# Performance work log

Hardware: AMD Instinct MI355X
Metric: run time of the kernel (lower is better)

The kernel has to match this reference:

```python
import jax, jax.numpy as jnp
import numpy as np

B, S, M, D, H = 2, 2048, 512, 1024, 16
HD = D // H      # head dim 64
KVC = D // 16    # MLA kv compression dim 64
QC = D // 32     # MLA q compression dim 32
RD = HD          # retrieval (qk) head dim 64
LOOKBACK = 8     # cross_window
EPS = 1e-6


def rmsnorm(x, w):
    return x * jax.lax.rsqrt(jnp.mean(x * x, axis=-1, keepdims=True) + EPS) * w


def setup_inputs():
    key = jax.random.key(0)
    ks = jax.random.split(key, 20)
    g = lambda i, shape: jax.random.normal(ks[i], shape, jnp.float32) * 0.02
    return {
        "x": jax.random.normal(ks[0], (B, S, D), jnp.float32),
        "memory": jax.random.normal(ks[1], (B, M, D), jnp.float32),
        "seg_ids": jnp.sort(jax.random.randint(ks[2], (B, S), 0, M), axis=-1),
        "norm1_w": jnp.ones((D,), jnp.float32),
        "W_dq": g(3, (D, QC)),
        "W_uq": g(4, (QC, H * RD)),
        "W_dkv": g(5, (D, KVC)),
        "W_uk": g(6, (KVC, H * RD)),
        "W_uv": g(7, (KVC, H * HD)),
        "W_o_self": g(8, (H * HD, D)),
        "norm2_w": jnp.ones((D,), jnp.float32),
        "W_q_c": g(9, (D, D)),
        "W_k_c": g(10, (D, D)),
        "W_v_c": g(11, (D, D)),
        "W_o_c": g(12, (D, D)),
        "norm3_w": jnp.ones((D,), jnp.float32),
        "W_gate": g(13, (D, 4 * D)),
        "W_up": g(14, (D, 4 * D)),
        "W_down": g(15, (4 * D, D)),
    }


def reference(x, memory, seg_ids, norm1_w, W_dq, W_uq, W_dkv, W_uk, W_uv,
              W_o_self, norm2_w, W_q_c, W_k_c, W_v_c, W_o_c, norm3_w,
              W_gate, W_up, W_down):
    # ---- MLA causal self-attention (low-rank compressed q/kv) ----
    h = rmsnorm(x, norm1_w)
    q = ((h @ W_dq) @ W_uq).reshape(B, S, H, RD)
    c_kv = h @ W_dkv                                  # [B,S,KVC]
    k = (c_kv @ W_uk).reshape(B, S, H, RD)
    v = (c_kv @ W_uv).reshape(B, S, H, HD)
    scores = jnp.einsum('bihd,bjhd->bhij', q, k) / np.float32(np.sqrt(RD))
    causal = jnp.tril(jnp.ones((S, S), bool))
    scores = jnp.where(causal, scores, -jnp.inf)
    attn = jax.nn.softmax(scores, axis=-1)
    o = jnp.einsum('bhij,bjhd->bihd', attn, v).reshape(B, S, H * HD)
    x = x + o @ W_o_self
    # ---- segment sliding-window cross-attention ----
    h = rmsnorm(x, norm2_w)
    qc = (h @ W_q_c).reshape(B, S, H, HD)
    kc = (memory @ W_k_c).reshape(B, M, H, HD)
    vc = (memory @ W_v_c).reshape(B, M, H, HD)
    sc = jnp.einsum('bihd,bjhd->bhij', qc, kc) / np.float32(np.sqrt(HD))
    kv_pos = jnp.arange(M)
    seg = seg_ids[:, :, None]                          # [B,S,1]
    allowed = (kv_pos[None, None, :] <= seg) & (kv_pos[None, None, :] >= seg - LOOKBACK)
    sc = jnp.where(allowed[:, None, :, :], sc, -jnp.inf)
    ac = jax.nn.softmax(sc, axis=-1)
    oc = jnp.einsum('bhij,bjhd->bihd', ac, vc).reshape(B, S, D)
    x = x + oc @ W_o_c
    # ---- SwiGLU FFN ----
    h = rmsnorm(x, norm3_w)
    x = x + (jax.nn.silu(h @ W_gate) * (h @ W_up)) @ W_down
    return x
```

## Files before the change

### kernel.cpp

```cpp
#include <hip/hip_runtime.h>
#include <stdint.h>

typedef unsigned short U16;
typedef __bf16 bf16x8 __attribute__((ext_vector_type(8)));
typedef unsigned short us8 __attribute__((ext_vector_type(8)));
typedef float f32x4 __attribute__((ext_vector_type(4)));

__device__ __forceinline__ U16 f2bf(float f) {
    unsigned u = __builtin_bit_cast(unsigned, f);
    unsigned r = (u + 0x7fff + ((u >> 16) & 1)) >> 16;
    return (U16)r;
}
__device__ __forceinline__ U16 f2bf_fast(float f) {
    return (U16)((__builtin_bit_cast(unsigned, f) + 0x8000u) >> 16);
}
__device__ __forceinline__ float bf2f(U16 v) {
    return __builtin_bit_cast(float, (unsigned)v << 16);
}
__device__ __forceinline__ bf16x8 ld8(const U16* p) { return __builtin_bit_cast(bf16x8, *(const us8*)p); }

__device__ __forceinline__ void async16(const U16* g, U16* l) {
    auto* gp = (const __attribute__((address_space(1))) U16*)g;
    auto* lp = (__attribute__((address_space(3))) U16*)(uintptr_t)(uint32_t)(uintptr_t)l;
    __builtin_amdgcn_global_load_lds(gp, lp, 16, 0, 0);
}

struct WEnt { const float* src; U16* dst; int K, N, Kpad, Npad, koff, noff, tiles; };
struct WTable { WEnt e[13]; };

__global__ __launch_bounds__(256) void wtrans_all(WTable t) {
    int bx = blockIdx.x, ei = 0;
    while (bx >= t.e[ei].tiles) { bx -= t.e[ei].tiles; ei++; }
    const WEnt E = t.e[ei];
    const int ntn = E.Npad >> 5;
    const int n0 = (bx % ntn) * 32, k0 = (bx / ntn) * 32;
    __shared__ float tile[32][33];
    const int tx = threadIdx.x & 31, ty = threadIdx.x >> 5;
#pragma unroll
    for (int i = 0; i < 4; i++) {
        int kk = k0 + ty + i * 8, n = n0 + tx;
        int k = kk - E.koff;
        float v = (k >= 0 && k < E.K && n < E.N) ? E.src[(size_t)k * E.N + n] : 0.f;
        tile[ty + i * 8][tx] = v;
    }
    __syncthreads();
#pragma unroll
    for (int i = 0; i < 4; i++) {
        int n = n0 + ty + i * 8, kk = k0 + tx;
        E.dst[(size_t)(E.noff + n) * E.Kpad + kk] = f2bf(tile[tx][ty + i * 8]);
    }
}

__global__ __launch_bounds__(256) void f2bf_k(const float* __restrict__ in, U16* __restrict__ out, int n) {
    int i = (blockIdx.x * 256 + threadIdx.x) * 4;
    if (i < n) {
        float4 v = *(const float4*)(in + i);
        out[i + 0] = f2bf(v.x); out[i + 1] = f2bf(v.y);
        out[i + 2] = f2bf(v.z); out[i + 3] = f2bf(v.w);
    }
}

__global__ __launch_bounds__(256) void cq_reduce(const float* __restrict__ p, U16* __restrict__ out) {
    int i = (blockIdx.x * 256 + threadIdx.x) * 4;
    const float4 a = *(const float4*)(p + i);
    const float4 b = *(const float4*)(p + 524288 + i);
    const float4 c = *(const float4*)(p + 2 * 524288 + i);
    const float4 d = *(const float4*)(p + 3 * 524288 + i);
    out[i + 0] = f2bf(a.x + b.x + c.x + d.x);
    out[i + 1] = f2bf(a.y + b.y + c.y + d.y);
    out[i + 2] = f2bf(a.z + b.z + c.z + d.z);
    out[i + 3] = f2bf(a.w + b.w + c.w + d.w);
}

__global__ __launch_bounds__(256) void rmsnorm_k(const float* __restrict__ x, const float* __restrict__ w,
                                                 U16* __restrict__ h) {
    const int row = blockIdx.x, tid = threadIdx.x;
    const float4 v = *(const float4*)(x + (size_t)row * 1024 + tid * 4);
    float ss = v.x * v.x + v.y * v.y + v.z * v.z + v.w * v.w;
#pragma unroll
    for (int o = 32; o > 0; o >>= 1) ss += __shfl_xor(ss, o);
    __shared__ float red[4];
    if ((tid & 63) == 0) red[tid >> 6] = ss;
    __syncthreads();
    float tot = red[0] + red[1] + red[2] + red[3];
    float sc = rsqrtf(tot * (1.0f / 1024.0f) + 1e-6f);
    const float4 wv = *(const float4*)(w + tid * 4);
    U16* hp = h + (size_t)row * 1024 + tid * 4;
    hp[0] = f2bf(v.x * sc * wv.x); hp[1] = f2bf(v.y * sc * wv.y);
    hp[2] = f2bf(v.z * sc * wv.z); hp[3] = f2bf(v.w * sc * wv.w);
}

__global__ __launch_bounds__(256) void qkuv_gemm(const U16* __restrict__ A, const U16* __restrict__ Wuqk,
                                                 const U16* __restrict__ Wuv,
                                                 U16* __restrict__ qkb, U16* __restrict__ vt) {
    __shared__ __align__(16) U16 As[2][128 * 32];
    __shared__ __align__(16) U16 Bs[2][128 * 32];
    __shared__ __align__(16) U16 Ts[4][64 * 80];
    const int tid = threadIdx.x;
    const bool isuv = blockIdx.x >= 16;
    const U16* Bt = isuv ? Wuv : Wuqk;
    const int n0 = (isuv ? blockIdx.x - 16 : blockIdx.x) * 128;
    const int m0 = blockIdx.y * 128;
    const int wave = tid >> 6, lane = tid & 63, l16 = lane & 15, quad = lane >> 4;
    const int wm = (wave >> 1) * 64, wn = (wave & 1) * 64;
    const int sr = lane >> 2, sc = (lane & 3) * 8;
    const U16* gA = A + (size_t)(m0 + wave * 32 + sr) * 128 + sc;
    const U16* gB = Bt + (size_t)(n0 + wave * 32 + sr) * 128 + sc;
    f32x4 acc[4][4] = {};
    for (int kt = 0; kt < 128; kt += 64) {
        __syncthreads();
#pragma unroll
        for (int p = 0; p < 2; p++) {
            const int o = kt + p * 32;
            async16(gA + o, &As[p][(wave * 32) * 32]);
            async16(gA + 16 * 128 + o, &As[p][(wave * 32 + 16) * 32]);
            async16(gB + o, &Bs[p][(wave * 32) * 32]);
            async16(gB + 16 * 128 + o, &Bs[p][(wave * 32 + 16) * 32]);
        }
        __syncthreads();
#pragma unroll
        for (int p = 0; p < 2; p++) {
            bf16x8 af[4], bfr[4];
#pragma unroll
            for (int i = 0; i < 4; i++) {
                af[i]  = ld8(&As[p][(wm + i * 16 + l16) * 32 + quad * 8]);
                bfr[i] = ld8(&Bs[p][(wn + i * 16 + l16) * 32 + quad * 8]);
            }
#pragma unroll
            for (int mi = 0; mi < 4; mi++)
#pragma unroll
                for (int ni = 0; ni < 4; ni++)
                    acc[mi][ni] = __builtin_amdgcn_mfma_f32_16x16x32_bf16(af[mi], bfr[ni], acc[mi][ni], 0, 0, 0);
        }
    }
    if (isuv) {
        U16* T = Ts[wave];
#pragma unroll
        for (int mi = 0; mi < 4; mi++)
#pragma unroll
            for (int ni = 0; ni < 4; ni++)
#pragma unroll
                for (int r = 0; r < 4; r++)
                    T[(ni * 16 + l16) * 80 + mi * 16 + quad * 4 + r] = f2bf(acc[mi][ni][r]);
#pragma unroll
        for (int c = 0; c < 8; c++) {
            int nloc = (lane >> 3) + 8 * c, mloc = (lane & 7) * 8;
            us8 v = *(const us8*)&T[nloc * 80 + mloc];
            *(us8*)&vt[(size_t)(n0 + wn + nloc) * 4096 + (m0 + wm + mloc)] = v;
        }
    } else {
#pragma unroll
        for (int mi = 0; mi < 4; mi++)
#pragma unroll
            for (int r = 0; r < 4; r++) {
                int m = m0 + wm + mi * 16 + quad * 4 + r;
#pragma unroll
                for (int ni = 0; ni < 4; ni++)
                    qkb[(size_t)m * 2048 + n0 + wn + ni * 16 + l16] = f2bf(acc[mi][ni][r]);
            }
    }
}

template <int EPI>
__global__ __launch_bounds__(256) void gemm_m64(const U16* __restrict__ A, const U16* __restrict__ Bt,
                                                void* __restrict__ Cout, const float* __restrict__ resid,
                                                int M, int N, int K, int lda, int ldb, int ldc) {
    __shared__ __align__(16) U16 As[4][64 * 32];
    __shared__ __align__(16) U16 Bs[4][128 * 32];
    const int tid = threadIdx.x;
    const int m0 = blockIdx.y * 64, n0 = blockIdx.x * 128;
    const int k0 = blockIdx.z * K;
    const int wave = tid >> 6, lane = tid & 63, l16 = lane & 15, quad = lane >> 4;
    const int wm = (wave >> 1) * 32, wn = (wave & 1) * 64;
    const int sr = lane >> 2, sc = (lane & 3) * 8;
    const U16* gA = A + (size_t)(m0 + wave * 16 + sr) * lda + sc + k0;
    const U16* gB = Bt + (size_t)(n0 + wave * 32 + sr) * ldb + sc + k0;
    f32x4 acc[2][4] = {};
    for (int kt = 0; kt < K; kt += 128) {
        __syncthreads();
#pragma unroll
        for (int p = 0; p < 4; p++) {
            const int o = kt + p * 32;
            async16(gA + o, &As[p][(wave * 16) * 32]);
            async16(gB + o, &Bs[p][(wave * 32) * 32]);
            async16(gB + (size_t)16 * ldb + o, &Bs[p][(wave * 32 + 16) * 32]);
        }
        __syncthreads();
#pragma unroll
        for (int p = 0; p < 4; p++) {
            bf16x8 af[2], bfr[4];
#pragma unroll
            for (int i = 0; i < 2; i++)
                af[i] = ld8(&As[p][(wm + i * 16 + l16) * 32 + quad * 8]);
#pragma unroll
            for (int i = 0; i < 4; i++)
                bfr[i] = ld8(&Bs[p][(wn + i * 16 + l16) * 32 + quad * 8]);
#pragma unroll
            for (int mi = 0; mi < 2; mi++)
#pragma unroll
                for (int ni = 0; ni < 4; ni++)
                    acc[mi][ni] = __builtin_amdgcn_mfma_f32_16x16x32_bf16(af[mi], bfr[ni], acc[mi][ni], 0, 0, 0);
        }
    }
#pragma unroll
    for (int mi = 0; mi < 2; mi++) {
#pragma unroll
        for (int r = 0; r < 4; r++) {
            int m = m0 + wm + mi * 16 + quad * 4 + r;
#pragma unroll
            for (int ni = 0; ni < 4; ni++) {
                int n = n0 + wn + ni * 16 + l16;
                float val = acc[mi][ni][r];
                if (EPI == 0) ((U16*)Cout)[(size_t)m * ldc + n] = f2bf(val);
                else if (EPI == 1) ((float*)Cout)[(size_t)m * ldc + n] = resid[(size_t)m * ldc + n] + val;
                else if (EPI == 5) ((float*)Cout)[(size_t)blockIdx.z * 524288 + (size_t)m * ldc + n] = val;
            }
        }
    }
}

__global__ __launch_bounds__(256) void qckv_gemm(const U16* __restrict__ hbuf, const U16* __restrict__ Wqc,
                                                 const U16* __restrict__ memb, const U16* __restrict__ Wkvc,
                                                 U16* __restrict__ qcb, U16* __restrict__ kvcb) {
    __shared__ __align__(16) U16 As[4][64 * 32];
    __shared__ __align__(16) U16 Bs[4][128 * 32];
    const int tid = threadIdx.x, bid = blockIdx.x;
    const U16 *A, *Bt; U16* C; int m0, n0, ldc;
    if (bid < 512) { A = hbuf; Bt = Wqc;  C = qcb;  m0 = (bid >> 3) * 64; n0 = (bid & 7) * 128;  ldc = 1024; }
    else { int b2 = bid - 512; A = memb; Bt = Wkvc; C = kvcb; m0 = (b2 >> 4) * 64; n0 = (b2 & 15) * 128; ldc = 2048; }
    const int wave = tid >> 6, lane = tid & 63, l16 = lane & 15, quad = lane >> 4;
    const int wm = (wave >> 1) * 32, wn = (wave & 1) * 64;
    const int sr = lane >> 2, sc = (lane & 3) * 8;
    const U16* gA = A + (size_t)(m0 + wave * 16 + sr) * 1024 + sc;
    const U16* gB = Bt + (size_t)(n0 + wave * 32 + sr) * 1024 + sc;
    f32x4 acc[2][4] = {};
    for (int kt = 0; kt < 1024; kt += 128) {
        __syncthreads();
#pragma unroll
        for (int p = 0; p < 4; p++) {
            const int o = kt + p * 32;
            async16(gA + o, &As[p][(wave * 16) * 32]);
            async16(gB + o, &Bs[p][(wave * 32) * 32]);
            async16(gB + 16 * 1024 + o, &Bs[p][(wave * 32 + 16) * 32]);
        }
        __syncthreads();
#pragma unroll
        for (int p = 0; p < 4; p++) {
            bf16x8 af[2], bfr[4];
#pragma unroll
            for (int i = 0; i < 2; i++)
                af[i] = ld8(&As[p][(wm + i * 16 + l16) * 32 + quad * 8]);
#pragma unroll
            for (int i = 0; i < 4; i++)
                bfr[i] = ld8(&Bs[p][(wn + i * 16 + l16) * 32 + quad * 8]);
#pragma unroll
            for (int mi = 0; mi < 2; mi++)
#pragma unroll
                for (int ni = 0; ni < 4; ni++)
                    acc[mi][ni] = __builtin_amdgcn_mfma_f32_16x16x32_bf16(af[mi], bfr[ni], acc[mi][ni], 0, 0, 0);
        }
    }
#pragma unroll
    for (int mi = 0; mi < 2; mi++)
#pragma unroll
        for (int r = 0; r < 4; r++) {
            int m = m0 + wm + mi * 16 + quad * 4 + r;
#pragma unroll
            for (int ni = 0; ni < 4; ni++)
                C[(size_t)m * ldc + n0 + wn + ni * 16 + l16] = f2bf(acc[mi][ni][r]);
        }
}

__global__ __launch_bounds__(512, 2) void ffn1_8ph(const U16* __restrict__ A, const U16* __restrict__ Wgu,
                                                   U16* __restrict__ Cout) {
    __shared__ __align__(16) U16 As[2][256 * 64];
    __shared__ __align__(16) U16 Bs[2][256 * 64];
    const int tid = threadIdx.x;
    const int wid = tid >> 6, lane = tid & 63;
    const int l16 = lane & 15, quad = lane >> 4;
    const int n0 = blockIdx.x * 128;
    const int m0 = blockIdx.y * 256;
    const int wr = wid >> 2, wc = wid & 3;
    const int wm = wr * 128;
    const int wn = wc * 64;
    const int srow = lane >> 3;
    const int schunk = (lane & 7) ^ srow;
    const U16* gA = A + (size_t)(m0 + wid * 32 + srow) * 1024 + schunk * 8;
    const U16* gB = Wgu + (size_t)((wid & 1) * 4096 + n0 + (wid >> 1) * 32 + srow) * 1024 + schunk * 8;

    auto STAGE = [&](int buf, int kt) {
        U16* la = &As[buf][(wid * 32) * 64];
        U16* lb = &Bs[buf][(wid * 32) * 64];
        const U16* pa = gA + kt;
        const U16* pb = gB + kt;
#pragma unroll
        for (int j = 0; j < 4; ++j) {
            async16(pa + j * 8 * 1024, la + j * 8 * 64);
            async16(pb + j * 8 * 1024, lb + j * 8 * 64);
        }
    };

    f32x4 acc[8][4] = {};

    auto TILE = [&](int buf) {
        const U16* Ab = &As[buf][0];
        const U16* Bb = &Bs[buf][0];
        const int cx = l16 & 7;
        bf16x8 a0[4][2], a1[4][2], b0[2][2], b1[2][2];
#pragma unroll
        for (int mi = 0; mi < 4; ++mi)
#pragma unroll
            for (int kh = 0; kh < 2; ++kh)
                a0[mi][kh] = ld8(&Ab[(wm + mi * 16 + l16) * 64 + (((kh * 4 + quad) ^ cx) << 3)]);
#pragma unroll
        for (int ni = 0; ni < 2; ++ni)
#pragma unroll
            for (int kh = 0; kh < 2; ++kh)
                b0[ni][kh] = ld8(&Bb[(wn + ni * 16 + l16) * 64 + (((kh * 4 + quad) ^ cx) << 3)]);
#pragma unroll
        for (int ni = 0; ni < 2; ++ni)
#pragma unroll
            for (int kh = 0; kh < 2; ++kh)
                b1[ni][kh] = ld8(&Bb[(wn + 32 + ni * 16 + l16) * 64 + (((kh * 4 + quad) ^ cx) << 3)]);
        __builtin_amdgcn_s_setprio(1);
#pragma unroll
        for (int mi = 0; mi < 4; ++mi)
#pragma unroll
            for (int ni = 0; ni < 2; ++ni)
#pragma unroll
                for (int kh = 0; kh < 2; ++kh)
                    acc[mi][ni] = __builtin_amdgcn_mfma_f32_16x16x32_bf16(a0[mi][kh], b0[ni][kh], acc[mi][ni], 0, 0, 0);
        __builtin_amdgcn_s_setprio(0);
#pragma unroll
        for (int mi = 0; mi < 4; ++mi)
#pragma unroll
            for (int kh = 0; kh < 2; ++kh)
                a1[mi][kh] = ld8(&Ab[(wm + 64 + mi * 16 + l16) * 64 + (((kh * 4 + quad) ^ cx) << 3)]);
        __builtin_amdgcn_s_setprio(1);
#pragma unroll
        for (int mi = 0; mi < 4; ++mi)
#pragma unroll
            for (int ni = 0; ni < 2; ++ni)
#pragma unroll
                for (int kh = 0; kh < 2; ++kh)
                    acc[mi][2 + ni] = __builtin_amdgcn_mfma_f32_16x16x32_bf16(a0[mi][kh], b1[ni][kh], acc[mi][2 + ni], 0, 0, 0);
        __builtin_amdgcn_s_setprio(0);
        __builtin_amdgcn_s_setprio(1);
#pragma unroll
        for (int mi = 0; mi < 4; ++mi)
#pragma unroll
            for (int ni = 0; ni < 2; ++ni)
#pragma unroll
                for (int kh = 0; kh < 2; ++kh)
                    acc[4 + mi][2 + ni] = __builtin_amdgcn_mfma_f32_16x16x32_bf16(a1[mi][kh], b1[ni][kh], acc[4 + mi][2 + ni], 0, 0, 0);
        __builtin_amdgcn_s_setprio(0);
        __builtin_amdgcn_s_setprio(1);
#pragma unroll
        for (int mi = 0; mi < 4; ++mi)
#pragma unroll
            for (int ni = 0; ni < 2; ++ni)
#pragma unroll
                for (int kh = 0; kh < 2; ++kh)
                    acc[4 + mi][ni] = __builtin_amdgcn_mfma_f32_16x16x32_bf16(a1[mi][kh], b0[ni][kh], acc[4 + mi][ni], 0, 0, 0);
        __builtin_amdgcn_s_setprio(0);
    };

    STAGE(0, 0);
    STAGE(1, 64);
#pragma unroll 1
    for (int t2 = 0; t2 < 7; ++t2) {
        asm volatile("s_waitcnt vmcnt(8)" ::: "memory");
        __builtin_amdgcn_s_barrier();
        __builtin_amdgcn_sched_barrier(0);
        TILE(0);
        __builtin_amdgcn_s_barrier();
        STAGE(0, (2 * t2 + 2) * 64);
        asm volatile("s_waitcnt vmcnt(8)" ::: "memory");
        __builtin_amdgcn_s_barrier();
        __builtin_amdgcn_sched_barrier(0);
        TILE(1);
        __builtin_amdgcn_s_barrier();
        STAGE(1, (2 * t2 + 3) * 64);
    }
    asm volatile("s_waitcnt vmcnt(8)" ::: "memory");
    __builtin_amdgcn_s_barrier();
    __builtin_amdgcn_sched_barrier(0);
    TILE(0);
    asm volatile("s_waitcnt vmcnt(0)" ::: "memory");
    __builtin_amdgcn_s_barrier();
    __builtin_amdgcn_sched_barrier(0);
    TILE(1);

#pragma unroll
    for (int mi = 0; mi < 8; ++mi)
#pragma unroll
        for (int r = 0; r < 4; ++r) {
            int m = m0 + wm + mi * 16 + quad * 4 + r;
#pragma unroll
            for (int ni = 0; ni < 2; ++ni) {
                int col = n0 + wc * 32 + ni * 16 + l16;
                float g = acc[mi][ni][r], u = acc[mi][ni + 2][r];
                float act = g / (1.f + __expf(-g)) * u;
                Cout[(size_t)m * 4096 + col] = f2bf(act);
            }
        }
}

__global__ __launch_bounds__(256) void flash_self3(const U16* __restrict__ QK, const U16* __restrict__ Vt,
                                                   U16* __restrict__ Og) {
    __shared__ __align__(16) U16 Ps[4 * 1280];
    __shared__ float Ored[4 * 2080];
    __shared__ float Lred[128];
    const int wave = threadIdx.x >> 6, lane = threadIdx.x & 63;
    const int l16 = lane & 15, quad = lane >> 4;
    const int bx = blockIdx.x;
    const int t = 63 - (bx >> 5);
    const int bh = bx & 31, b = bh >> 4, h = bh & 15;
    const int q0 = t * 32;
    const size_t rowQ0 = (size_t)(b * 2048 + q0 + l16) * 2048 + h * 64;
    const size_t rowQ1 = rowQ0 + 16 * 2048;
    bf16x8 aq[2][2];
    aq[0][0] = ld8(QK + rowQ0 + quad * 8);  aq[0][1] = ld8(QK + rowQ0 + 32 + quad * 8);
    aq[1][0] = ld8(QK + rowQ1 + quad * 8);  aq[1][1] = ld8(QK + rowQ1 + 32 + quad * 8);
    const U16* Kbase = QK + (size_t)(b * 2048) * 2048 + 1024 + h * 64;
    const U16* Vbase = Vt + (size_t)(h * 64) * 4096 + b * 2048;
    f32x4 o[2][4] = {};
    float ls[2][4] = {};
    U16* Pw = &Ps[wave * 1280];
    const int prd = l16 * 40 + ((quad ^ (l16 >> 2)) << 3);
    const int jend = q0 + 32;
    for (int j0 = wave * 32; j0 < jend; j0 += 128) {
        const U16* kp = Kbase + (size_t)j0 * 2048;
        bf16x8 b00 = ld8(kp + (size_t)l16 * 2048 + quad * 8);
        bf16x8 b01 = ld8(kp + (size_t)l16 * 2048 + 32 + quad * 8);
        bf16x8 b10 = ld8(kp + (size_t)(16 + l16) * 2048 + quad * 8);
        bf16x8 b11 = ld8(kp + (size_t)(16 + l16) * 2048 + 32 + quad * 8);
        bf16x8 v0 = ld8(Vbase + (size_t)(0  + l16) * 4096 + j0 + quad * 8);
        bf16x8 v1 = ld8(Vbase + (size_t)(16 + l16) * 4096 + j0 + quad * 8);
        bf16x8 v2 = ld8(Vbase + (size_t)(32 + l16) * 4096 + j0 + quad * 8);
        bf16x8 v3 = ld8(Vbase + (size_t)(48 + l16) * 4096 + j0 + quad * 8);
        f32x4 s[2][2] = {};
#pragma unroll
        for (int g = 0; g < 2; g++) {
            s[g][0] = __builtin_amdgcn_mfma_f32_16x16x32_bf16(aq[g][0], b00, s[g][0], 0, 0, 0);
            s[g][0] = __builtin_amdgcn_mfma_f32_16x16x32_bf16(aq[g][1], b01, s[g][0], 0, 0, 0);
            s[g][1] = __builtin_amdgcn_mfma_f32_16x16x32_bf16(aq[g][0], b10, s[g][1], 0, 0, 0);
            s[g][1] = __builtin_amdgcn_mfma_f32_16x16x32_bf16(aq[g][1], b11, s[g][1], 0, 0, 0);
        }
        float p0[2][4], p1[2][4];
        if (j0 + 32 >= jend) {
#pragma unroll
            for (int g = 0; g < 2; g++)
#pragma unroll
                for (int r = 0; r < 4; r++) {
                    int qg = q0 + g * 16 + quad * 4 + r;
                    p0[g][r] = (j0 + l16 <= qg) ? __expf(fminf(s[g][0][r] * 0.125f, 30.f)) : 0.f;
                    p1[g][r] = (j0 + 16 + l16 <= qg) ? __expf(fminf(s[g][1][r] * 0.125f, 30.f)) : 0.f;
                }
        } else {
#pragma unroll
            for (int g = 0; g < 2; g++)
#pragma unroll
                for (int r = 0; r < 4; r++) {
                    p0[g][r] = __expf(fminf(s[g][0][r] * 0.125f, 30.f));
                    p1[g][r] = __expf(fminf(s[g][1][r] * 0.125f, 30.f));
                }
        }
#pragma unroll
        for (int g = 0; g < 2; g++)
#pragma unroll
            for (int r = 0; r < 4; r++) {
                ls[g][r] += p0[g][r] + p1[g][r];
                int row = quad * 4 + r;
                Pw[g * 640 + row * 40 + ((((l16 >> 3) + 0) ^ quad) << 3) + (l16 & 7)] = f2bf_fast(p0[g][r]);
                Pw[g * 640 + row * 40 + ((((l16 >> 3) + 2) ^ quad) << 3) + (l16 & 7)] = f2bf_fast(p1[g][r]);
            }
#pragma unroll
        for (int g = 0; g < 2; g++) {
            bf16x8 ap = ld8(&Pw[g * 640 + prd]);
            o[g][0] = __builtin_amdgcn_mfma_f32_16x16x32_bf16(ap, v0, o[g][0], 0, 0, 0);
            o[g][1] = __builtin_amdgcn_mfma_f32_16x16x32_bf16(ap, v1, o[g][1], 0, 0, 0);
            o[g][2] = __builtin_amdgcn_mfma_f32_16x16x32_bf16(ap, v2, o[g][2], 0, 0, 0);
            o[g][3] = __builtin_amdgcn_mfma_f32_16x16x32_bf16(ap, v3, o[g][3], 0, 0, 0);
        }
    }
    float* Or = &Ored[wave * 2080];
#pragma unroll
    for (int g = 0; g < 2; g++) {
#pragma unroll
        for (int dg = 0; dg < 4; dg++)
#pragma unroll
            for (int r = 0; r < 4; r++)
                Or[(g * 16 + quad * 4 + r) * 65 + dg * 16 + l16] = o[g][dg][r];
#pragma unroll
        for (int r = 0; r < 4; r++) {
            float v = ls[g][r];
            v += __shfl_xor(v, 1); v += __shfl_xor(v, 2);
            v += __shfl_xor(v, 4); v += __shfl_xor(v, 8);
            if (l16 == 0) Lred[wave * 32 + g * 16 + quad * 4 + r] = v;
        }
    }
    __syncthreads();
    const int q = threadIdx.x >> 3, d0 = (threadIdx.x & 7) * 8;
    float l = Lred[q] + Lred[32 + q] + Lred[64 + q] + Lred[96 + q];
    float inv = 1.0f / l;
    us8 outv;
#pragma unroll
    for (int i = 0; i < 8; i++) {
        int idx = q * 65 + d0 + i;
        float s = Ored[idx] + Ored[2080 + idx] + Ored[4160 + idx] + Ored[6240 + idx];
        outv[i] = f2bf(s * inv);
    }
    *(us8*)(Og + (size_t)(b * 2048 + q0 + q) * 1024 + h * 64 + d0) = outv;
}

__global__ __launch_bounds__(256) void cross_attn(const U16* __restrict__ qc, const U16* __restrict__ kvc,
                                                  const int* __restrict__ seg_ids, U16* __restrict__ oc) {
    const int tok = blockIdx.x;
    const int b = tok >> 11;
    const int w = threadIdx.x >> 6, lane = threadIdx.x & 63;
    const int h = blockIdx.y * 4 + w;
    const int seg = seg_ids[tok];
    const size_t qoff = (size_t)tok * 1024 + h * 64 + lane;
    float q = bf2f(qc[qoff]);
    float s[9];
#pragma unroll
    for (int jj = 0; jj < 9; jj++) {
        int j = seg - 8 + jj;
        float sc = -INFINITY;
        if (j >= 0) {
            float kv = bf2f(kvc[((size_t)(b * 512) + j) * 2048 + h * 64 + lane]);
            sc = q * kv;
            sc += __shfl_xor(sc, 1); sc += __shfl_xor(sc, 2); sc += __shfl_xor(sc, 4);
            sc += __shfl_xor(sc, 8); sc += __shfl_xor(sc, 16); sc += __shfl_xor(sc, 32);
            sc *= 0.125f;
        }
        s[jj] = sc;
    }
    float m = s[0];
#pragma unroll
    for (int jj = 1; jj < 9; jj++) m = fmaxf(m, s[jj]);
    float l = 0.f, o = 0.f;
#pragma unroll
    for (int jj = 0; jj < 9; jj++) {
        int j = seg - 8 + jj;
        if (j >= 0) {
            float p = __expf(s[jj] - m);
            l += p;
            o += p * bf2f(kvc[((size_t)(b * 512) + j) * 2048 + 1024 + h * 64 + lane]);
        }
    }
    oc[qoff] = f2bf(o / l);
}

extern "C" void kernel_launch(void* const* d_in, const int* in_sizes, int n_in,
                              void* d_out, int out_size, void* d_ws, size_t ws_size,
                              hipStream_t stream) {
    const float* x      = (const float*)d_in[0];
    const float* memory = (const float*)d_in[1];
    const int*   seg    = (const int*)d_in[2];
    const float* n1w    = (const float*)d_in[3];
    const float* W_dq   = (const float*)d_in[4];
    const float* W_uq   = (const float*)d_in[5];
    const float* W_dkv  = (const float*)d_in[6];
    const float* W_uk   = (const float*)d_in[7];
    const float* W_uv   = (const float*)d_in[8];
    const float* W_os   = (const float*)d_in[9];
    const float* n2w    = (const float*)d_in[10];
    const float* W_qc   = (const float*)d_in[11];
    const float* W_kc   = (const float*)d_in[12];
    const float* W_vc   = (const float*)d_in[13];
    const float* W_oc   = (const float*)d_in[14];
    const float* n3w    = (const float*)d_in[15];
    const float* W_gate = (const float*)d_in[16];
    const float* W_up   = (const float*)d_in[17];
    const float* W_down = (const float*)d_in[18];
    (void)in_sizes; (void)n_in; (void)out_size; (void)ws_size;

    char* ws = (char*)d_ws;
    size_t off = 0;
    auto alloc = [&](size_t bytes) -> void* {
        void* p = ws + off;
        off += (bytes + 255) & ~(size_t)255;
        return p;
    };
    const size_t MB = 1024 * 1024;
    U16* hbuf     = (U16*)alloc(8 * MB);
    float* x1     = (float*)alloc(16 * MB);
    float* x2     = (float*)alloc(16 * MB);
    float* cq32   = (float*)alloc(8 * MB);
    U16* Wt_dqkv  = (U16*)alloc(128 * 1024 * 2);
    U16* Wt_uqk   = (U16*)alloc(2048 * 128 * 2);
    U16* Wt_uv    = (U16*)alloc(1024 * 128 * 2);
    U16* Wt_os    = (U16*)alloc(1024 * 1024 * 2);
    U16* Wt_qc    = (U16*)alloc(1024 * 1024 * 2);
    U16* Wt_kvc   = (U16*)alloc((size_t)2048 * 1024 * 2);
    U16* Wt_oc    = (U16*)alloc(1024 * 1024 * 2);
    U16* Wt_gu    = (U16*)alloc((size_t)8192 * 1024 * 2);
    U16* Wt_down  = (U16*)alloc((size_t)1024 * 4096 * 2);
    U16* mem_bf   = (U16*)alloc(1024 * 1024 * 2);
    char* arena   = ws + off;
    U16* cq  = (U16*)(arena);
    U16* qkb = (U16*)(arena + 1 * MB);
    U16* vt  = (U16*)(arena + 17 * MB);
    U16* ob  = (U16*)(arena + 25 * MB);
    U16* qcb  = (U16*)(arena);
    U16* kvcb = (U16*)(arena + 8 * MB);
    U16* ocb  = (U16*)(arena + 12 * MB);
    U16* gact = (U16*)(arena);

    WTable T;
    int i = 0;
    auto ent = [&](const float* s, U16* d, int K, int N, int Kpad, int Npad, int koff, int noff) {
        T.e[i++] = WEnt{s, d, K, N, Kpad, Npad, koff, noff, (Kpad >> 5) * (Npad >> 5)};
    };
    ent(W_dq,   Wt_dqkv, 1024, 32,   1024, 32,   0,  0);
    ent(W_dkv,  Wt_dqkv, 1024, 64,   1024, 96,   0,  32);
    ent(W_uq,   Wt_uqk,  32,   1024, 128,  1024, 0,  0);
    ent(W_uk,   Wt_uqk,  64,   1024, 128,  1024, 32, 1024);
    ent(W_uv,   Wt_uv,   64,   1024, 128,  1024, 32, 0);
    ent(W_os,   Wt_os,   1024, 1024, 1024, 1024, 0,  0);
    ent(W_qc,   Wt_qc,   1024, 1024, 1024, 1024, 0,  0);
    ent(W_kc,   Wt_kvc,  1024, 1024, 1024, 1024, 0,  0);
    ent(W_vc,   Wt_kvc,  1024, 1024, 1024, 1024, 0,  1024);
    ent(W_oc,   Wt_oc,   1024, 1024, 1024, 1024, 0,  0);
    ent(W_gate, Wt_gu,   1024, 4096, 1024, 4096, 0,  0);
    ent(W_up,   Wt_gu,   1024, 4096, 1024, 4096, 0,  4096);
    ent(W_down, Wt_down, 4096, 1024, 4096, 1024, 0,  0);
    int total_tiles = 0;
    for (int j = 0; j < 13; j++) total_tiles += T.e[j].tiles;
    wtrans_all<<<total_tiles, 256, 0, stream>>>(T);
    f2bf_k<<<1024, 256, 0, stream>>>(memory, mem_bf, 1024 * 1024);

    rmsnorm_k<<<4096, 256, 0, stream>>>(x, n1w, hbuf);
    gemm_m64<5><<<dim3(1, 64, 4), 256, 0, stream>>>(hbuf, Wt_dqkv, cq32, nullptr, 4096, 128, 256, 1024, 1024, 128);
    cq_reduce<<<512, 256, 0, stream>>>(cq32, cq);
    qkuv_gemm<<<dim3(24, 32), 256, 0, stream>>>(cq, Wt_uqk, Wt_uv, qkb, vt);
    flash_self3<<<2048, 256, 0, stream>>>(qkb, vt, ob);
    gemm_m64<1><<<dim3(8, 64), 256, 0, stream>>>(ob, Wt_os, x1, x, 4096, 1024, 1024, 1024, 1024, 1024);

    rmsnorm_k<<<4096, 256, 0, stream>>>(x1, n2w, hbuf);
    qckv_gemm<<<768, 256, 0, stream>>>(hbuf, Wt_qc, mem_bf, Wt_kvc, qcb, kvcb);
    cross_attn<<<dim3(4096, 4), 256, 0, stream>>>(qcb, kvcb, seg, ocb);
    gemm_m64<1><<<dim3(8, 64), 256, 0, stream>>>(ocb, Wt_oc, x2, x1, 4096, 1024, 1024, 1024, 1024, 1024);

    rmsnorm_k<<<4096, 256, 0, stream>>>(x2, n3w, hbuf);
    ffn1_8ph<<<dim3(32, 16), 512, 0, stream>>>(hbuf, Wt_gu, gact);
    gemm_m64<1><<<dim3(8, 64), 256, 0, stream>>>(gact, Wt_down, (float*)d_out, x2, 4096, 1024, 4096, 4096, 4096, 1024);
}
```

Before: 514.2 us.

## Software-pipeline self-attention over two KV tiles with MFMA priority and shared LDS

Each wave in the causal self-attention kernel now handles two 32-key tiles per iteration. The second tile's K/V loads and QK MFMAs are interleaved with the first tile's softmax and PV MFMAs, with s_setprio raised around the MFMA blocks. The P staging buffers and the output reduction buffer now share one LDS allocation, and launch bounds request 3 blocks per CU to raise occupancy. The aim is to hide global-load and exp latency behind matrix work, at the cost of more registers per thread.

```diff
diff --git a/kernel.cpp b/kernel.cpp
--- a/kernel.cpp
+++ b/kernel.cpp
@@ -406,11 +406,9 @@
         }
 }
 
-__global__ __launch_bounds__(256) void flash_self3(const U16* __restrict__ QK, const U16* __restrict__ Vt,
-                                                   U16* __restrict__ Og) {
-    __shared__ __align__(16) U16 Ps[4 * 1280];
-    __shared__ float Ored[4 * 2080];
-    __shared__ float Lred[128];
+__global__ __launch_bounds__(256, 3) void flash_self3(const U16* __restrict__ QK, const U16* __restrict__ Vt,
+                                                      U16* __restrict__ Og) {
+    __shared__ __align__(16) unsigned char SM[4 * 8320 + 512];
     const int wave = threadIdx.x >> 6, lane = threadIdx.x & 63;
     const int l16 = lane & 15, quad = lane >> 4;
     const int bx = blockIdx.x;
@@ -426,65 +424,140 @@
     const U16* Vbase = Vt + (size_t)(h * 64) * 4096 + b * 2048;
     f32x4 o[2][4] = {};
     float ls[2][4] = {};
-    U16* Pw = &Ps[wave * 1280];
+    U16* Pw = (U16*)(SM + wave * 8320);
+    float* LredP = (float*)(SM + 4 * 8320);
     const int prd = l16 * 40 + ((quad ^ (l16 >> 2)) << 3);
     const int jend = q0 + 32;
-    for (int j0 = wave * 32; j0 < jend; j0 += 128) {
-        const U16* kp = Kbase + (size_t)j0 * 2048;
-        bf16x8 b00 = ld8(kp + (size_t)l16 * 2048 + quad * 8);
-        bf16x8 b01 = ld8(kp + (size_t)l16 * 2048 + 32 + quad * 8);
-        bf16x8 b10 = ld8(kp + (size_t)(16 + l16) * 2048 + quad * 8);
-        bf16x8 b11 = ld8(kp + (size_t)(16 + l16) * 2048 + 32 + quad * 8);
-        bf16x8 v0 = ld8(Vbase + (size_t)(0  + l16) * 4096 + j0 + quad * 8);
-        bf16x8 v1 = ld8(Vbase + (size_t)(16 + l16) * 4096 + j0 + quad * 8);
-        bf16x8 v2 = ld8(Vbase + (size_t)(32 + l16) * 4096 + j0 + quad * 8);
-        bf16x8 v3 = ld8(Vbase + (size_t)(48 + l16) * 4096 + j0 + quad * 8);
-        f32x4 s[2][2] = {};
+    for (int j0 = wave * 32; j0 < jend; j0 += 256) {
+        const int jB = j0 + 128;
+        const bool hasB = jB < jend;
+        const U16* kpA = Kbase + (size_t)j0 * 2048;
+        bf16x8 ka0 = ld8(kpA + (size_t)l16 * 2048 + quad * 8);
+        bf16x8 ka1 = ld8(kpA + (size_t)l16 * 2048 + 32 + quad * 8);
+        bf16x8 ka2 = ld8(kpA + (size_t)(16 + l16) * 2048 + quad * 8);
+        bf16x8 ka3 = ld8(kpA + (size_t)(16 + l16) * 2048 + 32 + quad * 8);
+        bf16x8 va0 = ld8(Vbase + (size_t)(0  + l16) * 4096 + j0 + quad * 8);
+        bf16x8 va1 = ld8(Vbase + (size_t)(16 + l16) * 4096 + j0 + quad * 8);
+        bf16x8 va2 = ld8(Vbase + (size_t)(32 + l16) * 4096 + j0 + quad * 8);
+        bf16x8 va3 = ld8(Vbase + (size_t)(48 + l16) * 4096 + j0 + quad * 8);
+        bf16x8 kb0, kb1, kb2, kb3, vb0, vb1, vb2, vb3;
+        if (hasB) {
+            const U16* kpB = Kbase + (size_t)jB * 2048;
+            kb0 = ld8(kpB + (size_t)l16 * 2048 + quad * 8);
+            kb1 = ld8(kpB + (size_t)l16 * 2048 + 32 + quad * 8);
+            kb2 = ld8(kpB + (size_t)(16 + l16) * 2048 + quad * 8);
+            kb3 = ld8(kpB + (size_t)(16 + l16) * 2048 + 32 + quad * 8);
+        }
+        f32x4 sA[2][2] = {};
+        __builtin_amdgcn_s_setprio(1);
 #pragma unroll
         for (int g = 0; g < 2; g++) {
-            s[g][0] = __builtin_amdgcn_mfma_f32_16x16x32_bf16(aq[g][0], b00, s[g][0], 0, 0, 0);
-            s[g][0] = __builtin_amdgcn_mfma_f32_16x16x32_bf16(aq[g][1], b01, s[g][0], 0, 0, 0);
-            s[g][1] = __builtin_amdgcn_mfma_f32_16x16x32_bf16(aq[g][0], b10, s[g][1], 0, 0, 0);
-            s[g][1] = __builtin_amdgcn_mfma_f32_16x16x32_bf16(aq[g][1], b11, s[g][1], 0, 0, 0);
-        }
-        float p0[2][4], p1[2][4];
-        if (j0 + 32 >= jend) {
+            sA[g][0] = __builtin_amdgcn_mfma_f32_16x16x32_bf16(aq[g][0], ka0, sA[g][0], 0, 0, 0);
+            sA[g][0] = __builtin_amdgcn_mfma_f32_16x16x32_bf16(aq[g][1], ka1, sA[g][0], 0, 0, 0);
+            sA[g][1] = __builtin_amdgcn_mfma_f32_16x16x32_bf16(aq[g][0], ka2, sA[g][1], 0, 0, 0);
+            sA[g][1] = __builtin_amdgcn_mfma_f32_16x16x32_bf16(aq[g][1], ka3, sA[g][1], 0, 0, 0);
+        }
+        __builtin_amdgcn_s_setprio(0);
+        if (hasB) {
+            vb0 = ld8(Vbase + (size_t)(0  + l16) * 4096 + jB + quad * 8);
+            vb1 = ld8(Vbase + (size_t)(16 + l16) * 4096 + jB + quad * 8);
+            vb2 = ld8(Vbase + (size_t)(32 + l16) * 4096 + jB + quad * 8);
+            vb3 = ld8(Vbase + (size_t)(48 + l16) * 4096 + jB + quad * 8);
+        }
+        {
+            float p0[2][4], p1[2][4];
+            if (j0 + 32 >= jend) {
+#pragma unroll
+                for (int g = 0; g < 2; g++)
+#pragma unroll
+                    for (int r = 0; r < 4; r++) {
+                        int qg = q0 + g * 16 + quad * 4 + r;
+                        p0[g][r] = (j0 + l16 <= qg) ? __expf(fminf(sA[g][0][r] * 0.125f, 30.f)) : 0.f;
+                        p1[g][r] = (j0 + 16 + l16 <= qg) ? __expf(fminf(sA[g][1][r] * 0.125f, 30.f)) : 0.f;
+                    }
+            } else {
+#pragma unroll
+                for (int g = 0; g < 2; g++)
+#pragma unroll
+                    for (int r = 0; r < 4; r++) {
+                        p0[g][r] = __expf(fminf(sA[g][0][r] * 0.125f, 30.f));
+                        p1[g][r] = __expf(fminf(sA[g][1][r] * 0.125f, 30.f));
+                    }
+            }
 #pragma unroll
             for (int g = 0; g < 2; g++)
 #pragma unroll
                 for (int r = 0; r < 4; r++) {
-                    int qg = q0 + g * 16 + quad * 4 + r;
-                    p0[g][r] = (j0 + l16 <= qg) ? __expf(fminf(s[g][0][r] * 0.125f, 30.f)) : 0.f;
-                    p1[g][r] = (j0 + 16 + l16 <= qg) ? __expf(fminf(s[g][1][r] * 0.125f, 30.f)) : 0.f;
+                    ls[g][r] += p0[g][r] + p1[g][r];
+                    int row = quad * 4 + r;
+                    Pw[g * 640 + row * 40 + ((((l16 >> 3) + 0) ^ quad) << 3) + (l16 & 7)] = f2bf_fast(p0[g][r]);
+                    Pw[g * 640 + row * 40 + ((((l16 >> 3) + 2) ^ quad) << 3) + (l16 & 7)] = f2bf_fast(p1[g][r]);
                 }
-        } else {
-#pragma unroll
-            for (int g = 0; g < 2; g++)
-#pragma unroll
-                for (int r = 0; r < 4; r++) {
-                    p0[g][r] = __expf(fminf(s[g][0][r] * 0.125f, 30.f));
-                    p1[g][r] = __expf(fminf(s[g][1][r] * 0.125f, 30.f));
-                }
-        }
-#pragma unroll
-        for (int g = 0; g < 2; g++)
-#pragma unroll
-            for (int r = 0; r < 4; r++) {
-                ls[g][r] += p0[g][r] + p1[g][r];
-                int row = quad * 4 + r;
-                Pw[g * 640 + row * 40 + ((((l16 >> 3) + 0) ^ quad) << 3) + (l16 & 7)] = f2bf_fast(p0[g][r]);
-                Pw[g * 640 + row * 40 + ((((l16 >> 3) + 2) ^ quad) << 3) + (l16 & 7)] = f2bf_fast(p1[g][r]);
+        }
+        f32x4 sB[2][2] = {};
+        if (hasB) {
+            __builtin_amdgcn_s_setprio(1);
+#pragma unroll
+            for (int g = 0; g < 2; g++) {
+                sB[g][0] = __builtin_amdgcn_mfma_f32_16x16x32_bf16(aq[g][0], kb0, sB[g][0], 0, 0, 0);
+                sB[g][0] = __builtin_amdgcn_mfma_f32_16x16x32_bf16(aq[g][1], kb1, sB[g][0], 0, 0, 0);
+                sB[g][1] = __builtin_amdgcn_mfma_f32_16x16x32_bf16(aq[g][0], kb2, sB[g][1], 0, 0, 0);
+                sB[g][1] = __builtin_amdgcn_mfma_f32_16x16x32_bf16(aq[g][1], kb3, sB[g][1], 0, 0, 0);
             }
+            __builtin_amdgcn_s_setprio(0);
+        }
+        __builtin_amdgcn_s_setprio(1);
 #pragma unroll
         for (int g = 0; g < 2; g++) {
             bf16x8 ap = ld8(&Pw[g * 640 + prd]);
-            o[g][0] = __builtin_amdgcn_mfma_f32_16x16x32_bf16(ap, v0, o[g][0], 0, 0, 0);
-            o[g][1] = __builtin_amdgcn_mfma_f32_16x16x32_bf16(ap, v1, o[g][1], 0, 0, 0);
-            o[g][2] = __builtin_amdgcn_mfma_f32_16x16x32_bf16(ap, v2, o[g][2], 0, 0, 0);
-            o[g][3] = __builtin_amdgcn_mfma_f32_16x16x32_bf16(ap, v3, o[g][3], 0, 0, 0);
-        }
-    }
-    float* Or = &Ored[wave * 2080];
+            o[g][0] = __builtin_amdgcn_mfma_f32_16x16x32_bf16(ap, va0, o[g][0], 0, 0, 0);
+            o[g][1] = __builtin_amdgcn_mfma_f32_16x16x32_bf16(ap, va1, o[g][1], 0, 0, 0);
+            o[g][2] = __builtin_amdgcn_mfma_f32_16x16x32_bf16(ap, va2, o[g][2], 0, 0, 0);
+            o[g][3] = __builtin_amdgcn_mfma_f32_16x16x32_bf16(ap, va3, o[g][3], 0, 0, 0);
+        }
+        __builtin_amdgcn_s_setprio(0);
+        if (hasB) {
+            float p0[2][4], p1[2][4];
+            if (jB + 32 >= jend) {
+#pragma unroll
+                for (int g = 0; g < 2; g++)
+#pragma unroll
+                    for (int r = 0; r < 4; r++) {
+                        int qg = q0 + g * 16 + quad * 4 + r;
+                        p0[g][r] = (jB + l16 <= qg) ? __expf(fminf(sB[g][0][r] * 0.125f, 30.f)) : 0.f;
+                        p1[g][r] = (jB + 16 + l16 <= qg) ? __expf(fminf(sB[g][1][r] * 0.125f, 30.f)) : 0.f;
+                    }
+            } else {
+#pragma unroll
+                for (int g = 0; g < 2; g++)
+#pragma unroll
+                    for (int r = 0; r < 4; r++) {
+                        p0[g][r] = __expf(fminf(sB[g][0][r] * 0.125f, 30.f));
+                        p1[g][r] = __expf(fminf(sB[g][1][r] * 0.125f, 30.f));
+                    }
+            }
+#pragma unroll
+            for (int g = 0; g < 2; g++)
+#pragma unroll
+                for (int r = 0; r < 4; r++) {
+                    ls[g][r] += p0[g][r] + p1[g][r];
+                    int row = quad * 4 + r;
+                    Pw[1280 + g * 640 + row * 40 + ((((l16 >> 3) + 0) ^ quad) << 3) + (l16 & 7)] = f2bf_fast(p0[g][r]);
+                    Pw[1280 + g * 640 + row * 40 + ((((l16 >> 3) + 2) ^ quad) << 3) + (l16 & 7)] = f2bf_fast(p1[g][r]);
+                }
+            __builtin_amdgcn_s_setprio(1);
+#pragma unroll
+            for (int g = 0; g < 2; g++) {
+                bf16x8 ap = ld8(&Pw[1280 + g * 640 + prd]);
+                o[g][0] = __builtin_amdgcn_mfma_f32_16x16x32_bf16(ap, vb0, o[g][0], 0, 0, 0);
+                o[g][1] = __builtin_amdgcn_mfma_f32_16x16x32_bf16(ap, vb1, o[g][1], 0, 0, 0);
+                o[g][2] = __builtin_amdgcn_mfma_f32_16x16x32_bf16(ap, vb2, o[g][2], 0, 0, 0);
+                o[g][3] = __builtin_amdgcn_mfma_f32_16x16x32_bf16(ap, vb3, o[g][3], 0, 0, 0);
+            }
+            __builtin_amdgcn_s_setprio(0);
+        }
+    }
+    float* Or = (float*)SM + wave * 2080;
 #pragma unroll
     for (int g = 0; g < 2; g++) {
 #pragma unroll
@@ -497,18 +570,19 @@
             float v = ls[g][r];
             v += __shfl_xor(v, 1); v += __shfl_xor(v, 2);
             v += __shfl_xor(v, 4); v += __shfl_xor(v, 8);
-            if (l16 == 0) Lred[wave * 32 + g * 16 + quad * 4 + r] = v;
+            if (l16 == 0) LredP[wave * 32 + g * 16 + quad * 4 + r] = v;
         }
     }
     __syncthreads();
     const int q = threadIdx.x >> 3, d0 = (threadIdx.x & 7) * 8;
-    float l = Lred[q] + Lred[32 + q] + Lred[64 + q] + Lred[96 + q];
+    const float* OredA = (const float*)SM;
+    float l = LredP[q] + LredP[32 + q] + LredP[64 + q] + LredP[96 + q];
     float inv = 1.0f / l;
     us8 outv;
 #pragma unroll
     for (int i = 0; i < 8; i++) {
         int idx = q * 65 + d0 + i;
-        float s = Ored[idx] + Ored[2080 + idx] + Ored[4160 + idx] + Ored[6240 + idx];
+        float s = OredA[idx] + OredA[2080 + idx] + OredA[4160 + idx] + OredA[6240 + idx];
         outv[i] = f2bf(s * inv);
     }
     *(us8*)(Og + (size_t)(b * 2048 + q0 + q) * 1024 + h * 64 + d0) = outv;
```

Result: no change. 513.6 us (-0.1%).

## Restructure causal self-attention into 128-query blocks with shared LDS K/V double buffering

Applied to the files above, without the earlier changes.

The causal self-attention kernel now handles 128 queries per block instead of 32. Each wave owns two 16-row query groups and iterates over all key tiles. K and V tiles are staged into swizzled LDS with async global-to-LDS loads and double buffering, so all four waves share them instead of each wave loading K/V from global memory. This removes the cross-wave reduction of partial outputs through shared memory and lets waves skip fully masked tiles per query group. In exchange it adds barriers per tile and leaves the 32-row load imbalance of the causal triangle within a block.

```diff
diff --git a/kernel.cpp b/kernel.cpp
--- a/kernel.cpp
+++ b/kernel.cpp
@@ -406,112 +406,134 @@
         }
 }
 
-__global__ __launch_bounds__(256) void flash_self3(const U16* __restrict__ QK, const U16* __restrict__ Vt,
-                                                   U16* __restrict__ Og) {
-    __shared__ __align__(16) U16 Ps[4 * 1280];
-    __shared__ float Ored[4 * 2080];
-    __shared__ float Lred[128];
+__global__ __launch_bounds__(256, 3) void flash_self4(const U16* __restrict__ QK, const U16* __restrict__ Vt,
+                                                      U16* __restrict__ Og) {
+    __shared__ __align__(16) U16 Ks[2][32 * 64];
+    __shared__ __align__(16) U16 Vs[2][64 * 32];
+    __shared__ __align__(16) U16 Ps[4][1280];
     const int wave = threadIdx.x >> 6, lane = threadIdx.x & 63;
     const int l16 = lane & 15, quad = lane >> 4;
     const int bx = blockIdx.x;
-    const int t = 63 - (bx >> 5);
+    const int T = 15 - (bx >> 5);
     const int bh = bx & 31, b = bh >> 4, h = bh & 15;
-    const int q0 = t * 32;
-    const size_t rowQ0 = (size_t)(b * 2048 + q0 + l16) * 2048 + h * 64;
-    const size_t rowQ1 = rowQ0 + 16 * 2048;
+    const int q0 = T * 128;
+    const int NT = 4 * T + 4;
+    const int G0 = q0 + wave * 16, G1 = q0 + 64 + wave * 16;
     bf16x8 aq[2][2];
-    aq[0][0] = ld8(QK + rowQ0 + quad * 8);  aq[0][1] = ld8(QK + rowQ0 + 32 + quad * 8);
-    aq[1][0] = ld8(QK + rowQ1 + quad * 8);  aq[1][1] = ld8(QK + rowQ1 + 32 + quad * 8);
-    const U16* Kbase = QK + (size_t)(b * 2048) * 2048 + 1024 + h * 64;
-    const U16* Vbase = Vt + (size_t)(h * 64) * 4096 + b * 2048;
+    {
+        const size_t r0 = (size_t)(b * 2048 + G0 + l16) * 2048 + h * 64;
+        const size_t r1 = (size_t)(b * 2048 + G1 + l16) * 2048 + h * 64;
+        aq[0][0] = ld8(QK + r0 + quad * 8); aq[0][1] = ld8(QK + r0 + 32 + quad * 8);
+        aq[1][0] = ld8(QK + r1 + quad * 8); aq[1][1] = ld8(QK + r1 + 32 + quad * 8);
+    }
+    const int krow = wave * 8 + (lane >> 3);
+    const int kchunk = (lane & 7) ^ (lane >> 3);
+    const U16* gK = QK + (size_t)(b * 2048 + krow) * 2048 + 1024 + h * 64 + kchunk * 8;
+    const int vrow = wave * 16 + (lane >> 2);
+    const int vchunk = (lane & 3) ^ ((lane >> 2) & 3) ^ ((lane >> 4) & 3);
+    const U16* gV = Vt + (size_t)(h * 64 + vrow) * 4096 + b * 2048 + vchunk * 8;
+
+    auto STAGE = [&](int buf, int j0) {
+        async16(gK + (size_t)j0 * 2048, &Ks[buf][(wave * 8) * 64]);
+        async16(gV + j0, &Vs[buf][(wave * 16) * 32]);
+    };
+
     f32x4 o[2][4] = {};
     float ls[2][4] = {};
-    U16* Pw = &Ps[wave * 1280];
+    U16* Pw = Ps[wave];
     const int prd = l16 * 40 + ((quad ^ (l16 >> 2)) << 3);
-    const int jend = q0 + 32;
-    for (int j0 = wave * 32; j0 < jend; j0 += 128) {
-        const U16* kp = Kbase + (size_t)j0 * 2048;
-        bf16x8 b00 = ld8(kp + (size_t)l16 * 2048 + quad * 8);
-        bf16x8 b01 = ld8(kp + (size_t)l16 * 2048 + 32 + quad * 8);
-        bf16x8 b10 = ld8(kp + (size_t)(16 + l16) * 2048 + quad * 8);
-        bf16x8 b11 = ld8(kp + (size_t)(16 + l16) * 2048 + 32 + quad * 8);
-        bf16x8 v0 = ld8(Vbase + (size_t)(0  + l16) * 4096 + j0 + quad * 8);
-        bf16x8 v1 = ld8(Vbase + (size_t)(16 + l16) * 4096 + j0 + quad * 8);
-        bf16x8 v2 = ld8(Vbase + (size_t)(32 + l16) * 4096 + j0 + quad * 8);
-        bf16x8 v3 = ld8(Vbase + (size_t)(48 + l16) * 4096 + j0 + quad * 8);
-        f32x4 s[2][2] = {};
-#pragma unroll
-        for (int g = 0; g < 2; g++) {
-            s[g][0] = __builtin_amdgcn_mfma_f32_16x16x32_bf16(aq[g][0], b00, s[g][0], 0, 0, 0);
-            s[g][0] = __builtin_amdgcn_mfma_f32_16x16x32_bf16(aq[g][1], b01, s[g][0], 0, 0, 0);
-            s[g][1] = __builtin_amdgcn_mfma_f32_16x16x32_bf16(aq[g][0], b10, s[g][1], 0, 0, 0);
-            s[g][1] = __builtin_amdgcn_mfma_f32_16x16x32_bf16(aq[g][1], b11, s[g][1], 0, 0, 0);
-        }
-        float p0[2][4], p1[2][4];
-        if (j0 + 32 >= jend) {
-#pragma unroll
-            for (int g = 0; g < 2; g++)
-#pragma unroll
-                for (int r = 0; r < 4; r++) {
-                    int qg = q0 + g * 16 + quad * 4 + r;
-                    p0[g][r] = (j0 + l16 <= qg) ? __expf(fminf(s[g][0][r] * 0.125f, 30.f)) : 0.f;
-                    p1[g][r] = (j0 + 16 + l16 <= qg) ? __expf(fminf(s[g][1][r] * 0.125f, 30.f)) : 0.f;
+
+    auto TILE = [&](int buf, int j0) {
+        bf16x8 kf[2][2];
+#pragma unroll
+        for (int jh = 0; jh < 2; ++jh)
+#pragma unroll
+            for (int kh = 0; kh < 2; ++kh)
+                kf[jh][kh] = ld8(&Ks[buf][(jh * 16 + l16) * 64 + (((kh * 4 + quad) ^ (l16 & 7)) << 3)]);
+        bf16x8 vf[4];
+#pragma unroll
+        for (int dg = 0; dg < 4; ++dg)
+            vf[dg] = ld8(&Vs[buf][(dg * 16 + l16) * 32 + ((quad ^ (l16 & 3) ^ ((l16 >> 2) & 3)) << 3)]);
+#pragma unroll
+        for (int g = 0; g < 2; ++g) {
+            const int G = g ? G1 : G0;
+            if (j0 < G + 16) {
+                f32x4 s0 = {}, s1 = {};
+                __builtin_amdgcn_s_setprio(1);
+                s0 = __builtin_amdgcn_mfma_f32_16x16x32_bf16(aq[g][0], kf[0][0], s0, 0, 0, 0);
+                s0 = __builtin_amdgcn_mfma_f32_16x16x32_bf16(aq[g][1], kf[0][1], s0, 0, 0, 0);
+                s1 = __builtin_amdgcn_mfma_f32_16x16x32_bf16(aq[g][0], kf[1][0], s1, 0, 0, 0);
+                s1 = __builtin_amdgcn_mfma_f32_16x16x32_bf16(aq[g][1], kf[1][1], s1, 0, 0, 0);
+                __builtin_amdgcn_s_setprio(0);
+                float p0[4], p1[4];
+                if (j0 + 32 > G) {
+#pragma unroll
+                    for (int r = 0; r < 4; ++r) {
+                        int qg = G + quad * 4 + r;
+                        p0[r] = (j0 + l16 <= qg) ? __expf(fminf(s0[r] * 0.125f, 30.f)) : 0.f;
+                        p1[r] = (j0 + 16 + l16 <= qg) ? __expf(fminf(s1[r] * 0.125f, 30.f)) : 0.f;
+                    }
+                } else {
+#pragma unroll
+                    for (int r = 0; r < 4; ++r) {
+                        p0[r] = __expf(fminf(s0[r] * 0.125f, 30.f));
+                        p1[r] = __expf(fminf(s1[r] * 0.125f, 30.f));
+                    }
                 }
-        } else {
-#pragma unroll
-            for (int g = 0; g < 2; g++)
-#pragma unroll
-                for (int r = 0; r < 4; r++) {
-                    p0[g][r] = __expf(fminf(s[g][0][r] * 0.125f, 30.f));
-                    p1[g][r] = __expf(fminf(s[g][1][r] * 0.125f, 30.f));
+#pragma unroll
+                for (int r = 0; r < 4; ++r) {
+                    ls[g][r] += p0[r] + p1[r];
+                    int row = quad * 4 + r;
+                    Pw[g * 640 + row * 40 + ((((l16 >> 3) + 0) ^ quad) << 3) + (l16 & 7)] = f2bf_fast(p0[r]);
+                    Pw[g * 640 + row * 40 + ((((l16 >> 3) + 2) ^ quad) << 3) + (l16 & 7)] = f2bf_fast(p1[r]);
                 }
-        }
-#pragma unroll
-        for (int g = 0; g < 2; g++)
-#pragma unroll
-            for (int r = 0; r < 4; r++) {
-                ls[g][r] += p0[g][r] + p1[g][r];
-                int row = quad * 4 + r;
-                Pw[g * 640 + row * 40 + ((((l16 >> 3) + 0) ^ quad) << 3) + (l16 & 7)] = f2bf_fast(p0[g][r]);
-                Pw[g * 640 + row * 40 + ((((l16 >> 3) + 2) ^ quad) << 3) + (l16 & 7)] = f2bf_fast(p1[g][r]);
+                bf16x8 ap = ld8(&Pw[g * 640 + prd]);
+                __builtin_amdgcn_s_setprio(1);
+                o[g][0] = __builtin_amdgcn_mfma_f32_16x16x32_bf16(ap, vf[0], o[g][0], 0, 0, 0);
+                o[g][1] = __builtin_amdgcn_mfma_f32_16x16x32_bf16(ap, vf[1], o[g][1], 0, 0, 0);
+                o[g][2] = __builtin_amdgcn_mfma_f32_16x16x32_bf16(ap, vf[2], o[g][2], 0, 0, 0);
+                o[g][3] = __builtin_amdgcn_mfma_f32_16x16x32_bf16(ap, vf[3], o[g][3], 0, 0, 0);
+                __builtin_amdgcn_s_setprio(0);
             }
-#pragma unroll
-        for (int g = 0; g < 2; g++) {
-            bf16x8 ap = ld8(&Pw[g * 640 + prd]);
-            o[g][0] = __builtin_amdgcn_mfma_f32_16x16x32_bf16(ap, v0, o[g][0], 0, 0, 0);
-            o[g][1] = __builtin_amdgcn_mfma_f32_16x16x32_bf16(ap, v1, o[g][1], 0, 0, 0);
-            o[g][2] = __builtin_amdgcn_mfma_f32_16x16x32_bf16(ap, v2, o[g][2], 0, 0, 0);
-            o[g][3] = __builtin_amdgcn_mfma_f32_16x16x32_bf16(ap, v3, o[g][3], 0, 0, 0);
-        }
-    }
-    float* Or = &Ored[wave * 2080];
-#pragma unroll
-    for (int g = 0; g < 2; g++) {
-#pragma unroll
-        for (int dg = 0; dg < 4; dg++)
-#pragma unroll
-            for (int r = 0; r < 4; r++)
-                Or[(g * 16 + quad * 4 + r) * 65 + dg * 16 + l16] = o[g][dg][r];
-#pragma unroll
-        for (int r = 0; r < 4; r++) {
+        }
+    };
+
+    STAGE(0, 0);
+    STAGE(1, 32);
+#pragma unroll 1
+    for (int it = 0; it < NT - 2; ++it) {
+        asm volatile("s_waitcnt vmcnt(2)" ::: "memory");
+        __builtin_amdgcn_s_barrier();
+        __builtin_amdgcn_sched_barrier(0);
+        TILE(it & 1, it * 32);
+        __builtin_amdgcn_s_barrier();
+        STAGE(it & 1, (it + 2) * 32);
+    }
+    asm volatile("s_waitcnt vmcnt(2)" ::: "memory");
+    __builtin_amdgcn_s_barrier();
+    __builtin_amdgcn_sched_barrier(0);
+    TILE(NT & 1, (NT - 2) * 32);
+    asm volatile("s_waitcnt vmcnt(0)" ::: "memory");
+    __builtin_amdgcn_s_barrier();
+    __builtin_amdgcn_sched_barrier(0);
+    TILE((NT - 1) & 1, (NT - 1) * 32);
+
+#pragma unroll
+    for (int g = 0; g < 2; ++g) {
+        const int G = g ? G1 : G0;
+#pragma unroll
+        for (int r = 0; r < 4; ++r) {
             float v = ls[g][r];
             v += __shfl_xor(v, 1); v += __shfl_xor(v, 2);
             v += __shfl_xor(v, 4); v += __shfl_xor(v, 8);
-            if (l16 == 0) Lred[wave * 32 + g * 16 + quad * 4 + r] = v;
-        }
-    }
-    __syncthreads();
-    const int q = threadIdx.x >> 3, d0 = (threadIdx.x & 7) * 8;
-    float l = Lred[q] + Lred[32 + q] + Lred[64 + q] + Lred[96 + q];
-    float inv = 1.0f / l;
-    us8 outv;
-#pragma unroll
-    for (int i = 0; i < 8; i++) {
-        int idx = q * 65 + d0 + i;
-        float s = Ored[idx] + Ored[2080 + idx] + Ored[4160 + idx] + Ored[6240 + idx];
-        outv[i] = f2bf(s * inv);
-    }
-    *(us8*)(Og + (size_t)(b * 2048 + q0 + q) * 1024 + h * 64 + d0) = outv;
+            float inv = 1.0f / v;
+            int qrow = G + quad * 4 + r;
+            U16* op = Og + (size_t)(b * 2048 + qrow) * 1024 + h * 64 + l16;
+#pragma unroll
+            for (int dg = 0; dg < 4; ++dg)
+                op[dg * 16] = f2bf(o[g][dg][r] * inv);
+        }
+    }
 }
 
 __global__ __launch_bounds__(256) void cross_attn(const U16* __restrict__ qc, const U16* __restrict__ kvc,
@@ -636,7 +658,7 @@
     gemm_m64<5><<<dim3(1, 64, 4), 256, 0, stream>>>(hbuf, Wt_dqkv, cq32, nullptr, 4096, 128, 256, 1024, 1024, 128);
     cq_reduce<<<512, 256, 0, stream>>>(cq32, cq);
     qkuv_gemm<<<dim3(24, 32), 256, 0, stream>>>(cq, Wt_uqk, Wt_uv, qkb, vt);
-    flash_self3<<<2048, 256, 0, stream>>>(qkb, vt, ob);
+    flash_self4<<<512, 256, 0, stream>>>(qkb, vt, ob);
     gemm_m64<1><<<dim3(8, 64), 256, 0, stream>>>(ob, Wt_os, x1, x, 4096, 1024, 1024, 1024, 1024, 1024);
 
     rmsnorm_k<<<4096, 256, 0, stream>>>(x1, n2w, hbuf);
```

Measured after the change: 499.6 us. -2.8%, faster.
